# Optimization experiments

Measured on AMD Instinct MI355X. Metric: run time of the kernel, lower is better.

The kernel has to match this reference:

```python
import jax, jax.numpy as jnp
import numpy as np

B, N, D = 2, 2048, 512
H, DH = 8, 64
P = 64  # position_max_embedding


def setup_inputs() -> dict:
    key = jax.random.key(0)
    ks = jax.random.split(key, 8)
    s = 0.02
    return {
        "x": jax.random.normal(ks[0], (B, N, D), jnp.float32),
        "Wq": jax.random.normal(ks[1], (D, H * DH), jnp.float32) * s,
        "Wk": jax.random.normal(ks[2], (D, H * DH), jnp.float32) * s,
        "Wv": jax.random.normal(ks[3], (D, H * DH), jnp.float32) * s,
        "rel_pos": jax.random.normal(ks[4], (2 * P + 1, H), jnp.float32) * s,
        "c_emb": jax.random.uniform(ks[5], (2 * P + 1, H), jnp.float32, 0.5, 1.5),
        "Wo": jax.random.normal(ks[6], (H * DH, D), jnp.float32) * s,
        "bo": jnp.zeros((D,), jnp.float32),
    }


def reference(x, Wq, Wk, Wv, rel_pos, c_emb, Wo, bo):
    b, n, _ = x.shape
    scale = DH ** -0.5
    q = (x @ Wq).reshape(b, n, H, DH)
    k = (x @ Wk).reshape(b, n, H, DH)
    v = (x @ Wv).reshape(b, n, H, DH)
    # relative position index: j - i, clamped to [-P, P], shifted to [0, 2P]
    idx = jnp.clip(jnp.arange(n)[None, :] - jnp.arange(n)[:, None], -P, P) + P  # [n, n]
    pos_bias = rel_pos[idx]          # [n, n, H]
    c_gate = c_emb[idx]              # [n, n, H]
    sim = jnp.einsum('bihd,bjhd->bhij', q, k)  # [b, H, n, n]
    sim = (sim + pos_bias.transpose(2, 0, 1)[None]) * scale
    attn = jax.nn.softmax(sim, axis=-1) * c_gate.transpose(2, 0, 1)[None]
    out = jnp.einsum('bhij,bjhd->bihd', attn, v).reshape(b, n, H * DH)
    return out @ Wo + bo
```

## Files before the change

kernel.cpp:

```cpp
#include <hip/hip_runtime.h>
#include <hip/hip_bf16.h>
#include <stdint.h>

#define BB 2
#define NN 2048
#define DD 512
#define HH 8
#define DHH 64

typedef __attribute__((ext_vector_type(8))) short bf16x8;
typedef __attribute__((ext_vector_type(4))) float f32x4;

#define LOG2E 1.44269504088896340736f

#if __has_builtin(__builtin_amdgcn_exp2f)
#define QSCALE (0.125f * LOG2E)
#define EXP2(x) __builtin_amdgcn_exp2f(x)
#else
#define QSCALE 0.125f
#define EXP2(x) __expf(x)
#endif

static __device__ __forceinline__ unsigned short f2bf(float f) {
    union { float f; unsigned u; } v; v.f = f;
    unsigned r = v.u + 0x7fffu + ((v.u >> 16) & 1u);
    return (unsigned short)(r >> 16);
}

static __device__ __forceinline__ unsigned pk2(float a, float b) {
    __hip_bfloat162 h = __float22bfloat162_rn(make_float2(a, b));
    union { __hip_bfloat162 h; unsigned u; } cv; cv.h = h;
    return cv.u;
}

static __device__ __forceinline__ bf16x8 ld8(const unsigned short* p) {
    bf16x8 v; __builtin_memcpy(&v, p, 16); return v;
}

static __device__ __forceinline__ void gld_lds16(const void* g, void* l) {
    __builtin_amdgcn_global_load_lds((const __attribute__((address_space(1))) void*)g,
                                     (__attribute__((address_space(3))) void*)l, 16, 0, 0);
}

__global__ void ca_prep(const float* __restrict__ x,
                        const float* __restrict__ w0, const float* __restrict__ w1,
                        const float* __restrict__ w2, const float* __restrict__ w3,
                        unsigned short* __restrict__ xb, unsigned short* __restrict__ wts) {
    __shared__ float T[64][65];
    int bx = blockIdx.x;
    if (bx < 2048) {
        int gid = bx * 256 + threadIdx.x;
        float4 v = ((const float4*)x)[gid];
        ushort4 o;
        o.x = f2bf(v.x); o.y = f2bf(v.y); o.z = f2bf(v.z); o.w = f2bf(v.w);
        ((ushort4*)xb)[gid] = o;
        return;
    }
    int bb = bx - 2048;
    int z = bb >> 6, t = bb & 63;
    const float* W = (z == 0) ? w0 : (z == 1) ? w1 : (z == 2) ? w2 : w3;
    unsigned short* out = wts + z * 262144;
    int k0 = (t & 7) << 6, n0 = (t >> 3) << 6;
    int c = threadIdx.x & 63, r4 = threadIdx.x >> 6;
#pragma unroll
    for (int rr = 0; rr < 16; ++rr) {
        int r = r4 * 16 + rr;
        T[r][c] = W[(k0 + r) * 512 + n0 + c];
    }
    __syncthreads();
#pragma unroll
    for (int rr = 0; rr < 16; ++rr) {
        int r = r4 * 16 + rr;
        out[(n0 + r) * 512 + k0 + c] = f2bf(T[c][r]);
    }
}

__global__ __launch_bounds__(256, 3)
void ca_gemm_proj(const unsigned short* __restrict__ A,
                  const unsigned short* __restrict__ wts,
                  unsigned short* __restrict__ qkv,
                  unsigned short* __restrict__ vt) {
    __shared__ __align__(16) unsigned short Ash[2][128 * 64];
    __shared__ __align__(16) unsigned short Bsh[2][64 * 64];
    int z = blockIdx.y >> 3;
    const unsigned short* BT = wts + z * 262144;
    unsigned short* out = qkv + z * 2097152;
    int w = threadIdx.x >> 6, lane = threadIdx.x & 63;
    int c = lane & 15, qd = lane >> 4;
    int m0 = blockIdx.x * 128 + w * 16;
    int n0 = (blockIdx.y & 7) * 64;

    int lr = lane >> 3, ls = lane & 7;
    int soff = lr * 512 + ((ls ^ (lr & 7)) << 3);
    const unsigned short* Ab = A + (blockIdx.x * 128) * 512 + soff;
    const unsigned short* Bb = BT + n0 * 512 + soff;

#pragma unroll
    for (int L = 0; L < 4; ++L)
        gld_lds16(Ab + (w * 32 + L * 8) * 512, (char*)Ash[0] + (w * 32 + L * 8) * 128);
#pragma unroll
    for (int L = 0; L < 2; ++L)
        gld_lds16(Bb + (w * 16 + L * 8) * 512, (char*)Bsh[0] + (w * 16 + L * 8) * 128);

    f32x4 acc[2][4];
#pragma unroll
    for (int mt = 0; mt < 2; ++mt)
#pragma unroll
        for (int nb = 0; nb < 4; ++nb) acc[mt][nb] = (f32x4){0.f, 0.f, 0.f, 0.f};

    int cs = c & 7;
#pragma unroll
    for (int k = 0; k < 8; ++k) {
        int b = k & 1;
        if (k < 7) {
            int k0 = (k + 1) * 64;
#pragma unroll
            for (int L = 0; L < 4; ++L)
                gld_lds16(Ab + k0 + (w * 32 + L * 8) * 512, (char*)Ash[b ^ 1] + (w * 32 + L * 8) * 128);
#pragma unroll
            for (int L = 0; L < 2; ++L)
                gld_lds16(Bb + k0 + (w * 16 + L * 8) * 512, (char*)Bsh[b ^ 1] + (w * 16 + L * 8) * 128);
            asm volatile("s_waitcnt vmcnt(6)" ::: "memory");
        } else {
            asm volatile("s_waitcnt vmcnt(0)" ::: "memory");
        }
        __syncthreads();
        bf16x8 a[2][2], bq[4][2];
#pragma unroll
        for (int mt = 0; mt < 2; ++mt)
#pragma unroll
            for (int kk = 0; kk < 2; ++kk)
                a[mt][kk] = ld8((const unsigned short*)((char*)Ash[b] +
                                (w * 16 + mt * 64 + c) * 128 + (((kk * 4 + qd) ^ cs) << 4)));
#pragma unroll
        for (int nb = 0; nb < 4; ++nb)
#pragma unroll
            for (int kk = 0; kk < 2; ++kk)
                bq[nb][kk] = ld8((const unsigned short*)((char*)Bsh[b] +
                                (nb * 16 + c) * 128 + (((kk * 4 + qd) ^ cs) << 4)));
        asm volatile("s_waitcnt lgkmcnt(0)" ::: "memory");
        __syncthreads();
#pragma unroll
        for (int kk = 0; kk < 2; ++kk)
#pragma unroll
            for (int nb = 0; nb < 4; ++nb) {
                acc[0][nb] = __builtin_amdgcn_mfma_f32_16x16x32_bf16(a[0][kk], bq[nb][kk], acc[0][nb], 0, 0, 0);
                acc[1][nb] = __builtin_amdgcn_mfma_f32_16x16x32_bf16(a[1][kk], bq[nb][kk], acc[1][nb], 0, 0, 0);
            }
    }

    if (z == 2) {
#pragma unroll
        for (int mt = 0; mt < 2; ++mt) {
            int ib = m0 + mt * 64 + qd * 4;
            int b = ib >> 11, i = ib & 2047;
#pragma unroll
            for (int nb = 0; nb < 4; ++nb) {
                int col = n0 + nb * 16 + c;
                int h = col >> 6, d = col & 63;
                ushort4 pk;
                pk.x = f2bf(acc[mt][nb][0]); pk.y = f2bf(acc[mt][nb][1]);
                pk.z = f2bf(acc[mt][nb][2]); pk.w = f2bf(acc[mt][nb][3]);
                *(ushort4*)(vt + (((b << 3) + h) * 64 + d) * 2048 + i) = pk;
            }
        }
    } else {
        float scale = (z == 0) ? QSCALE : 1.0f;
#pragma unroll
        for (int mt = 0; mt < 2; ++mt)
#pragma unroll
            for (int nb = 0; nb < 4; ++nb) {
#pragma unroll
                for (int r = 0; r < 4; ++r) {
                    int row = m0 + mt * 64 + qd * 4 + r;
                    int col = n0 + nb * 16 + c;
                    int b = row >> 11, i = row & 2047, h = col >> 6, d = col & 63;
                    out[(((b << 3) + h) * 2048 + i) * 64 + d] = f2bf(acc[mt][nb][r] * scale);
                }
            }
    }
}

__global__ __launch_bounds__(256, 4)
void ca_flash(const unsigned short* __restrict__ Q,
              const unsigned short* __restrict__ K,
              const unsigned short* __restrict__ VT,
              const float* __restrict__ rel_pos,
              const float* __restrict__ c_emb,
              unsigned short* __restrict__ Ob) {
    __shared__ __align__(16) char smem[37904];
    unsigned (*Ptu)[16][16] = (unsigned (*)[16][16])(smem + 32768);
    float* red = (float*)smem;
    float2* lrg = (float2*)(smem + 36864);

    int bx = blockIdx.x;
    int xcd = bx & 7, slot = bx >> 3;
    int bh = xcd + ((slot >> 6) << 3);
    int it = slot & 63;
    int b = bh >> 3, h = bh & 7;
    int w = threadIdx.x >> 6, lane = threadIdx.x & 63;
    int c = lane & 15, qd = lane >> 4;
    int i0 = it * 32;

    if (threadIdx.x < 129) {
        lrg[threadIdx.x] = make_float2(rel_pos[threadIdx.x * 8 + h] * QSCALE,
                                       c_emb[threadIdx.x * 8 + h]);
    }

    const unsigned short* Qh = Q  + bh * 131072;
    const unsigned short* Kh = K  + bh * 131072;
    const unsigned short* Vh = VT + bh * 131072;
    char* kw = smem + w * 4096;
    char* vw = smem + 16384 + w * 4096;

    int koff[4], voff[4];
#pragma unroll
    for (int L = 0; L < 4; ++L) {
        int kr = L * 8 + (lane >> 3);
        koff[L] = kr * 64 + (((lane & 7) ^ ((kr >> 1) & 7)) << 3);
        int vr = L * 16 + (lane >> 2);
        voff[L] = vr * 2048 + (((lane & 3) ^ ((lane >> 3) & 3)) << 3);
    }

    {
        int j0 = w * 32;
#pragma unroll
        for (int L = 0; L < 4; ++L) gld_lds16(Kh + j0 * 64 + koff[L], kw + L * 1024);
#pragma unroll
        for (int L = 0; L < 4; ++L) gld_lds16(Vh + j0 + voff[L], vw + L * 1024);
    }

    bf16x8 aq[2][2];
#pragma unroll
    for (int qt = 0; qt < 2; ++qt) {
        aq[qt][0] = ld8(Qh + (i0 + qt * 16 + c) * 64 + qd * 8);
        aq[qt][1] = ld8(Qh + (i0 + qt * 16 + c) * 64 + 32 + qd * 8);
    }

    f32x4 o2[2][4];
    float lp2[2][4];
#pragma unroll
    for (int qt = 0; qt < 2; ++qt)
#pragma unroll
        for (int db = 0; db < 4; ++db) {
            o2[qt][db] = (f32x4){0.f, 0.f, 0.f, 0.f};
            lp2[qt][db] = 0.f;
        }

    __syncthreads();

    int ksw  = c & 7;
    int vsw  = (c >> 1) & 3;

    for (int t = 0; t < 16; ++t) {
        asm volatile("s_waitcnt vmcnt(4)" ::: "memory");
        __builtin_amdgcn_sched_barrier(0);
        bf16x8 bk0a = ld8((const unsigned short*)(kw + (2 * c) * 128     + (((qd)     ^ ksw) << 4)));
        bf16x8 bk0b = ld8((const unsigned short*)(kw + (2 * c) * 128     + (((qd + 4) ^ ksw) << 4)));
        bf16x8 bk1a = ld8((const unsigned short*)(kw + (2 * c + 1) * 128 + (((qd)     ^ ksw) << 4)));
        bf16x8 bk1b = ld8((const unsigned short*)(kw + (2 * c + 1) * 128 + (((qd + 4) ^ ksw) << 4)));
        asm volatile("s_waitcnt vmcnt(0)" ::: "memory");
        __builtin_amdgcn_sched_barrier(0);
        bf16x8 bv[4];
#pragma unroll
        for (int db = 0; db < 4; ++db)
            bv[db] = ld8((const unsigned short*)(vw + (db * 16 + c) * 64 + ((qd ^ vsw) << 4)));
        asm volatile("s_waitcnt lgkmcnt(0)" ::: "memory");
        __builtin_amdgcn_sched_barrier(0);
        if (t < 15) {
            int j0n = ((t + 1) * 4 + w) * 32;
#pragma unroll
            for (int L = 0; L < 4; ++L) gld_lds16(Kh + j0n * 64 + koff[L], kw + L * 1024);
#pragma unroll
            for (int L = 0; L < 4; ++L) gld_lds16(Vh + j0n + voff[L], vw + L * 1024);
        }

        int j0 = (t * 4 + w) * 32;

        f32x4 s[2][2];
        __builtin_amdgcn_s_setprio(1);
#pragma unroll
        for (int qt = 0; qt < 2; ++qt) {
            s[qt][0] = (f32x4){0.f, 0.f, 0.f, 0.f};
            s[qt][1] = (f32x4){0.f, 0.f, 0.f, 0.f};
            s[qt][0] = __builtin_amdgcn_mfma_f32_16x16x32_bf16(aq[qt][0], bk0a, s[qt][0], 0, 0, 0);
            s[qt][1] = __builtin_amdgcn_mfma_f32_16x16x32_bf16(aq[qt][0], bk1a, s[qt][1], 0, 0, 0);
            s[qt][0] = __builtin_amdgcn_mfma_f32_16x16x32_bf16(aq[qt][1], bk0b, s[qt][0], 0, 0, 0);
            s[qt][1] = __builtin_amdgcn_mfma_f32_16x16x32_bf16(aq[qt][1], bk1b, s[qt][1], 0, 0, 0);
        }
        __builtin_amdgcn_s_setprio(0);

#pragma unroll
        for (int qt = 0; qt < 2; ++qt) {
            int iqt0 = i0 + qt * 16;
            int iq = iqt0 + qd * 4;
            bool lowc  = (j0 + 31 - iqt0) <= -64;
            bool highc = (j0 - (iqt0 + 15)) >= 64;
            if (lowc || highc) {
                int d = lowc ? 0 : 128;
                float2 gg = lrg[d];
#pragma unroll
                for (int r = 0; r < 4; ++r) {
                    float t0 = EXP2(s[qt][0][r] + gg.x);
                    float t1 = EXP2(s[qt][1][r] + gg.x);
                    lp2[qt][r] += t0 + t1;
                    Ptu[w][qd * 4 + r][c] = pk2(t0 * gg.y, t1 * gg.y);
                }
            } else {
#pragma unroll
                for (int r = 0; r < 4; ++r) {
                    int i = iq + r;
                    int j = j0 + 2 * c;
                    int d0 = j - i;     d0 = (d0 < -64) ? -64 : (d0 > 64 ? 64 : d0); d0 += 64;
                    int d1 = j + 1 - i; d1 = (d1 < -64) ? -64 : (d1 > 64 ? 64 : d1); d1 += 64;
                    float2 g0 = lrg[d0];
                    float2 g1 = lrg[d1];
                    float t0 = EXP2(s[qt][0][r] + g0.x);
                    float t1 = EXP2(s[qt][1][r] + g1.x);
                    lp2[qt][r] += t0 + t1;
                    Ptu[w][qd * 4 + r][c] = pk2(t0 * g0.y, t1 * g1.y);
                }
            }
            bf16x8 ap = ld8((const unsigned short*)&Ptu[w][c][0] + qd * 8);
            __builtin_amdgcn_s_setprio(1);
#pragma unroll
            for (int db = 0; db < 4; ++db)
                o2[qt][db] = __builtin_amdgcn_mfma_f32_16x16x32_bf16(ap, bv[db], o2[qt][db], 0, 0, 0);
            __builtin_amdgcn_s_setprio(0);
        }
    }

    __syncthreads();
    if (w > 0) {
        float* dst = red + (w - 1) * (64 * 41) + lane * 41;
#pragma unroll
        for (int qt = 0; qt < 2; ++qt)
#pragma unroll
            for (int db = 0; db < 4; ++db)
#pragma unroll
                for (int r = 0; r < 4; ++r)
                    dst[qt * 16 + db * 4 + r] = o2[qt][db][r];
#pragma unroll
        for (int qt = 0; qt < 2; ++qt)
#pragma unroll
            for (int r = 0; r < 4; ++r)
                dst[32 + qt * 4 + r] = lp2[qt][r];
    }
    __syncthreads();
    if (w == 0) {
#pragma unroll
        for (int ww = 0; ww < 3; ++ww) {
            const float* src = red + ww * (64 * 41) + lane * 41;
#pragma unroll
            for (int qt = 0; qt < 2; ++qt) {
#pragma unroll
                for (int db = 0; db < 4; ++db)
#pragma unroll
                    for (int r = 0; r < 4; ++r)
                        o2[qt][db][r] += src[qt * 16 + db * 4 + r];
#pragma unroll
                for (int r = 0; r < 4; ++r)
                    lp2[qt][r] += src[32 + qt * 4 + r];
            }
        }
#pragma unroll
        for (int qt = 0; qt < 2; ++qt)
#pragma unroll
            for (int r = 0; r < 4; ++r) {
                lp2[qt][r] += __shfl_xor(lp2[qt][r], 1);
                lp2[qt][r] += __shfl_xor(lp2[qt][r], 2);
                lp2[qt][r] += __shfl_xor(lp2[qt][r], 4);
                lp2[qt][r] += __shfl_xor(lp2[qt][r], 8);
            }
#pragma unroll
        for (int qt = 0; qt < 2; ++qt)
#pragma unroll
            for (int db = 0; db < 4; ++db)
#pragma unroll
                for (int r = 0; r < 4; ++r) {
                    int row = b * 2048 + i0 + qt * 16 + qd * 4 + r;
                    int col = h * 64 + db * 16 + c;
                    Ob[row * 512 + col] = f2bf(o2[qt][db][r] / lp2[qt][r]);
                }
    }
}

__global__ __launch_bounds__(256, 4)
void ca_gemm_out(const unsigned short* __restrict__ A,
                 const unsigned short* __restrict__ BT,
                 const float* __restrict__ bias,
                 float* __restrict__ out) {
    __shared__ __align__(16) unsigned short Ash[2][64 * 64];
    __shared__ __align__(16) unsigned short Bsh[2][64 * 64];
    int w = threadIdx.x >> 6, lane = threadIdx.x & 63;
    int c = lane & 15, qd = lane >> 4;
    int m0 = blockIdx.x * 64 + w * 16;
    int n0 = blockIdx.y * 64;

    int lr = lane >> 3, ls = lane & 7;
    int soff = lr * 512 + ((ls ^ (lr & 7)) << 3);
    const unsigned short* Ab = A + (blockIdx.x * 64) * 512 + soff;
    const unsigned short* Bb = BT + n0 * 512 + soff;

#pragma unroll
    for (int L = 0; L < 2; ++L) {
        gld_lds16(Ab + (w * 16 + L * 8) * 512, (char*)Ash[0] + (w * 16 + L * 8) * 128);
        gld_lds16(Bb + (w * 16 + L * 8) * 512, (char*)Bsh[0] + (w * 16 + L * 8) * 128);
    }

    f32x4 acc[4];
#pragma unroll
    for (int nb = 0; nb < 4; ++nb) acc[nb] = (f32x4){0.f, 0.f, 0.f, 0.f};

    int cs = c & 7;
#pragma unroll
    for (int k = 0; k < 8; ++k) {
        int b = k & 1;
        if (k < 7) {
            int k0 = (k + 1) * 64;
#pragma unroll
            for (int L = 0; L < 2; ++L) {
                gld_lds16(Ab + k0 + (w * 16 + L * 8) * 512, (char*)Ash[b ^ 1] + (w * 16 + L * 8) * 128);
                gld_lds16(Bb + k0 + (w * 16 + L * 8) * 512, (char*)Bsh[b ^ 1] + (w * 16 + L * 8) * 128);
            }
            asm volatile("s_waitcnt vmcnt(4)" ::: "memory");
        } else {
            asm volatile("s_waitcnt vmcnt(0)" ::: "memory");
        }
        __syncthreads();
        bf16x8 a[2], bq[4][2];
#pragma unroll
        for (int kk = 0; kk < 2; ++kk)
            a[kk] = ld8((const unsigned short*)((char*)Ash[b] +
                        (w * 16 + c) * 128 + (((kk * 4 + qd) ^ cs) << 4)));
#pragma unroll
        for (int nb = 0; nb < 4; ++nb)
#pragma unroll
            for (int kk = 0; kk < 2; ++kk)
                bq[nb][kk] = ld8((const unsigned short*)((char*)Bsh[b] +
                                (nb * 16 + c) * 128 + (((kk * 4 + qd) ^ cs) << 4)));
        asm volatile("s_waitcnt lgkmcnt(0)" ::: "memory");
        __syncthreads();
#pragma unroll
        for (int kk = 0; kk < 2; ++kk)
#pragma unroll
            for (int nb = 0; nb < 4; ++nb)
                acc[nb] = __builtin_amdgcn_mfma_f32_16x16x32_bf16(a[kk], bq[nb][kk], acc[nb], 0, 0, 0);
    }
#pragma unroll
    for (int nb = 0; nb < 4; ++nb) {
#pragma unroll
        for (int r = 0; r < 4; ++r) {
            int row = m0 + qd * 4 + r;
            int col = n0 + nb * 16 + c;
            out[row * 512 + col] = acc[nb][r] + bias[col];
        }
    }
}

extern "C" void kernel_launch(void* const* d_in, const int* in_sizes, int n_in,
                              void* d_out, int out_size, void* d_ws, size_t ws_size,
                              hipStream_t stream) {
    const float* x   = (const float*)d_in[0];
    const float* Wq  = (const float*)d_in[1];
    const float* Wk  = (const float*)d_in[2];
    const float* Wv  = (const float*)d_in[3];
    const float* rel = (const float*)d_in[4];
    const float* cem = (const float*)d_in[5];
    const float* Wo  = (const float*)d_in[6];
    const float* bo  = (const float*)d_in[7];
    float* out = (float*)d_out;
    char* ws = (char*)d_ws;

    unsigned short* xb  = (unsigned short*)(ws);
    unsigned short* wts = (unsigned short*)(ws + 4194304);
    unsigned short* qkv = (unsigned short*)(ws + 6291456);
    unsigned short* vt  = (unsigned short*)(ws + 18874368);
    unsigned short* ob  = (unsigned short*)(ws + 23068672);

    hipLaunchKernelGGL(ca_prep, dim3(2304), dim3(256), 0, stream, x, Wq, Wk, Wv, Wo, xb, wts);
    hipLaunchKernelGGL(ca_gemm_proj, dim3(32, 24), dim3(256), 0, stream, xb, wts, qkv, vt);
    hipLaunchKernelGGL(ca_flash, dim3(1024), dim3(256), 0, stream,
                       qkv, qkv + 2097152, vt, rel, cem, ob);
    hipLaunchKernelGGL(ca_gemm_out, dim3(64, 8), dim3(256), 0, stream, ob, wts + 3 * 262144, bo, out);
}
```

Measured before the change: 136.6 us.

## Fuse fp32-to-bf16 conversion into QKV projection and move Wo transpose into flash

```diff
diff --git a/kernel.cpp b/kernel.cpp
--- a/kernel.cpp
+++ b/kernel.cpp
@@ -42,65 +42,34 @@
                                      (__attribute__((address_space(3))) void*)l, 16, 0, 0);
 }
 
-__global__ void ca_prep(const float* __restrict__ x,
-                        const float* __restrict__ w0, const float* __restrict__ w1,
-                        const float* __restrict__ w2, const float* __restrict__ w3,
-                        unsigned short* __restrict__ xb, unsigned short* __restrict__ wts) {
-    __shared__ float T[64][65];
-    int bx = blockIdx.x;
-    if (bx < 2048) {
-        int gid = bx * 256 + threadIdx.x;
-        float4 v = ((const float4*)x)[gid];
-        ushort4 o;
-        o.x = f2bf(v.x); o.y = f2bf(v.y); o.z = f2bf(v.z); o.w = f2bf(v.w);
-        ((ushort4*)xb)[gid] = o;
-        return;
-    }
-    int bb = bx - 2048;
-    int z = bb >> 6, t = bb & 63;
-    const float* W = (z == 0) ? w0 : (z == 1) ? w1 : (z == 2) ? w2 : w3;
-    unsigned short* out = wts + z * 262144;
-    int k0 = (t & 7) << 6, n0 = (t >> 3) << 6;
-    int c = threadIdx.x & 63, r4 = threadIdx.x >> 6;
-#pragma unroll
-    for (int rr = 0; rr < 16; ++rr) {
-        int r = r4 * 16 + rr;
-        T[r][c] = W[(k0 + r) * 512 + n0 + c];
-    }
-    __syncthreads();
-#pragma unroll
-    for (int rr = 0; rr < 16; ++rr) {
-        int r = r4 * 16 + rr;
-        out[(n0 + r) * 512 + k0 + c] = f2bf(T[c][r]);
-    }
-}
-
 __global__ __launch_bounds__(256, 3)
-void ca_gemm_proj(const unsigned short* __restrict__ A,
-                  const unsigned short* __restrict__ wts,
-                  unsigned short* __restrict__ qkv,
-                  unsigned short* __restrict__ vt) {
-    __shared__ __align__(16) unsigned short Ash[2][128 * 64];
-    __shared__ __align__(16) unsigned short Bsh[2][64 * 64];
+void ca_projf(const float* __restrict__ x,
+              const float* __restrict__ w0, const float* __restrict__ w1,
+              const float* __restrict__ w2,
+              unsigned short* __restrict__ qkv,
+              unsigned short* __restrict__ vt) {
+    __shared__ __align__(16) unsigned short Ash[128 * 64];
+    __shared__ __align__(16) unsigned short Bsh[64 * 64];
     int z = blockIdx.y >> 3;
-    const unsigned short* BT = wts + z * 262144;
+    const float* W = (z == 0) ? w0 : (z == 1) ? w1 : w2;
     unsigned short* out = qkv + z * 2097152;
-    int w = threadIdx.x >> 6, lane = threadIdx.x & 63;
+    int tid = threadIdx.x;
+    int w = tid >> 6, lane = tid & 63;
     int c = lane & 15, qd = lane >> 4;
     int m0 = blockIdx.x * 128 + w * 16;
     int n0 = (blockIdx.y & 7) * 64;
 
-    int lr = lane >> 3, ls = lane & 7;
-    int soff = lr * 512 + ((ls ^ (lr & 7)) << 3);
-    const unsigned short* Ab = A + (blockIdx.x * 128) * 512 + soff;
-    const unsigned short* Bb = BT + n0 * 512 + soff;
-
-#pragma unroll
-    for (int L = 0; L < 4; ++L)
-        gld_lds16(Ab + (w * 32 + L * 8) * 512, (char*)Ash[0] + (w * 32 + L * 8) * 128);
-#pragma unroll
-    for (int L = 0; L < 2; ++L)
-        gld_lds16(Bb + (w * 16 + L * 8) * 512, (char*)Bsh[0] + (w * 16 + L * 8) * 128);
+    int rowA = tid >> 1, ha = tid & 1;
+    const float* xA = x + (blockIdx.x * 128 + rowA) * 512 + ha * 32;
+    int nB = tid >> 2, kq = tid & 3;
+    const float* wB = W + n0 + nB;
+
+    float4 fA4[8];
+    float  fB[16];
+#pragma unroll
+    for (int j = 0; j < 8; ++j) fA4[j] = *(const float4*)(xA + j * 4);
+#pragma unroll
+    for (int j = 0; j < 16; ++j) fB[j] = wB[(kq * 16 + j) * 512];
 
     f32x4 acc[2][4];
 #pragma unroll
@@ -109,37 +78,51 @@
         for (int nb = 0; nb < 4; ++nb) acc[mt][nb] = (f32x4){0.f, 0.f, 0.f, 0.f};
 
     int cs = c & 7;
-#pragma unroll
+    int ra7 = rowA & 7, nb7 = nB & 7;
     for (int k = 0; k < 8; ++k) {
-        int b = k & 1;
+        asm volatile("s_waitcnt vmcnt(0)" ::: "memory");
+        __syncthreads();
+#pragma unroll
+        for (int q = 0; q < 4; ++q) {
+            uint4 pkk;
+            pkk.x = pk2(fA4[q * 2].x, fA4[q * 2].y);
+            pkk.y = pk2(fA4[q * 2].z, fA4[q * 2].w);
+            pkk.z = pk2(fA4[q * 2 + 1].x, fA4[q * 2 + 1].y);
+            pkk.w = pk2(fA4[q * 2 + 1].z, fA4[q * 2 + 1].w);
+            int sl = (ha * 4 + q) ^ ra7;
+            *(uint4*)((char*)Ash + rowA * 128 + sl * 16) = pkk;
+        }
+#pragma unroll
+        for (int q = 0; q < 2; ++q) {
+            uint4 pkk;
+            pkk.x = pk2(fB[q * 8 + 0], fB[q * 8 + 1]);
+            pkk.y = pk2(fB[q * 8 + 2], fB[q * 8 + 3]);
+            pkk.z = pk2(fB[q * 8 + 4], fB[q * 8 + 5]);
+            pkk.w = pk2(fB[q * 8 + 6], fB[q * 8 + 7]);
+            int sl = (kq * 2 + q) ^ nb7;
+            *(uint4*)((char*)Bsh + nB * 128 + sl * 16) = pkk;
+        }
+        __syncthreads();
         if (k < 7) {
-            int k0 = (k + 1) * 64;
-#pragma unroll
-            for (int L = 0; L < 4; ++L)
-                gld_lds16(Ab + k0 + (w * 32 + L * 8) * 512, (char*)Ash[b ^ 1] + (w * 32 + L * 8) * 128);
-#pragma unroll
-            for (int L = 0; L < 2; ++L)
-                gld_lds16(Bb + k0 + (w * 16 + L * 8) * 512, (char*)Bsh[b ^ 1] + (w * 16 + L * 8) * 128);
-            asm volatile("s_waitcnt vmcnt(6)" ::: "memory");
-        } else {
-            asm volatile("s_waitcnt vmcnt(0)" ::: "memory");
-        }
-        __syncthreads();
+            int k0n = (k + 1) * 64;
+#pragma unroll
+            for (int j = 0; j < 8; ++j) fA4[j] = *(const float4*)(xA + k0n + j * 4);
+#pragma unroll
+            for (int j = 0; j < 16; ++j) fB[j] = wB[(k0n + kq * 16 + j) * 512];
+        }
         bf16x8 a[2][2], bq[4][2];
 #pragma unroll
         for (int mt = 0; mt < 2; ++mt)
 #pragma unroll
             for (int kk = 0; kk < 2; ++kk)
-                a[mt][kk] = ld8((const unsigned short*)((char*)Ash[b] +
+                a[mt][kk] = ld8((const unsigned short*)((char*)Ash +
                                 (w * 16 + mt * 64 + c) * 128 + (((kk * 4 + qd) ^ cs) << 4)));
 #pragma unroll
         for (int nb = 0; nb < 4; ++nb)
 #pragma unroll
             for (int kk = 0; kk < 2; ++kk)
-                bq[nb][kk] = ld8((const unsigned short*)((char*)Bsh[b] +
+                bq[nb][kk] = ld8((const unsigned short*)((char*)Bsh +
                                 (nb * 16 + c) * 128 + (((kk * 4 + qd) ^ cs) << 4)));
-        asm volatile("s_waitcnt lgkmcnt(0)" ::: "memory");
-        __syncthreads();
 #pragma unroll
         for (int kk = 0; kk < 2; ++kk)
 #pragma unroll
@@ -187,13 +170,35 @@
               const unsigned short* __restrict__ VT,
               const float* __restrict__ rel_pos,
               const float* __restrict__ c_emb,
-              unsigned short* __restrict__ Ob) {
+              unsigned short* __restrict__ Ob,
+              const float* __restrict__ Wo,
+              unsigned short* __restrict__ woT) {
     __shared__ __align__(16) char smem[37904];
+
+    if (blockIdx.x < 64) {
+        float (*T)[65] = (float (*)[65])smem;
+        int t = blockIdx.x;
+        int k0 = (t & 7) << 6, n0 = (t >> 3) << 6;
+        int c = threadIdx.x & 63, r4 = threadIdx.x >> 6;
+#pragma unroll
+        for (int rr = 0; rr < 16; ++rr) {
+            int r = r4 * 16 + rr;
+            T[r][c] = Wo[(k0 + r) * 512 + n0 + c];
+        }
+        __syncthreads();
+#pragma unroll
+        for (int rr = 0; rr < 16; ++rr) {
+            int r = r4 * 16 + rr;
+            woT[(n0 + r) * 512 + k0 + c] = f2bf(T[c][r]);
+        }
+        return;
+    }
+
     unsigned (*Ptu)[16][16] = (unsigned (*)[16][16])(smem + 32768);
     float* red = (float*)smem;
     float2* lrg = (float2*)(smem + 36864);
 
-    int bx = blockIdx.x;
+    int bx = blockIdx.x - 64;
     int xcd = bx & 7, slot = bx >> 3;
     int bh = xcd + ((slot >> 6) << 3);
     int it = slot & 63;
@@ -472,15 +477,13 @@
     float* out = (float*)d_out;
     char* ws = (char*)d_ws;
 
-    unsigned short* xb  = (unsigned short*)(ws);
-    unsigned short* wts = (unsigned short*)(ws + 4194304);
+    unsigned short* woT = (unsigned short*)(ws + 4194304);
     unsigned short* qkv = (unsigned short*)(ws + 6291456);
     unsigned short* vt  = (unsigned short*)(ws + 18874368);
     unsigned short* ob  = (unsigned short*)(ws + 23068672);
 
-    hipLaunchKernelGGL(ca_prep, dim3(2304), dim3(256), 0, stream, x, Wq, Wk, Wv, Wo, xb, wts);
-    hipLaunchKernelGGL(ca_gemm_proj, dim3(32, 24), dim3(256), 0, stream, xb, wts, qkv, vt);
-    hipLaunchKernelGGL(ca_flash, dim3(1024), dim3(256), 0, stream,
-                       qkv, qkv + 2097152, vt, rel, cem, ob);
-    hipLaunchKernelGGL(ca_gemm_out, dim3(64, 8), dim3(256), 0, stream, ob, wts + 3 * 262144, bo, out);
-}
+    hipLaunchKernelGGL(ca_projf, dim3(32, 24), dim3(256), 0, stream, x, Wq, Wk, Wv, qkv, vt);
+    hipLaunchKernelGGL(ca_flash, dim3(1088), dim3(256), 0, stream,
+                       qkv, qkv + 2097152, vt, rel, cem, ob, Wo, woT);
+    hipLaunchKernelGGL(ca_gemm_out, dim3(64, 8), dim3(256), 0, stream, ob, woT, bo, out);
+}
```

After: 159.3 us. 1.17x slower.
